# Kernel optimization log

Hardware: AMD Instinct MI355X
Metric: run time of the kernel (lower is better)

Reference implementation:

```python
import jax, jax.numpy as jnp
import numpy as np

PATCH = 16
STRIDE = 8  # patch_size - overlap

def setup_inputs() -> dict:
    key = jax.random.key(0)
    x = jax.random.normal(key, (16, 3, 512, 512), dtype=jnp.float32)
    return {"x": x, "k_neighbors": 8}

def reference(x, k_neighbors):
    B, C, H, W = x.shape
    p, s = PATCH, STRIDE
    nh = (H - p) // s + 1
    nw = (W - p) // s + 1
    N = nh * nw
    # F.unfold equivalent: feature dim ordered (C, kh, kw), then transpose(1,2)
    patches = jax.lax.conv_general_dilated_patches(
        x, filter_shape=(p, p), window_strides=(s, s), padding='VALID')  # [B, C*p*p, nh, nw]
    patches = patches.reshape(B, C * p * p, N).transpose(0, 2, 1)  # [B, N, C*p*p]
    # grid positions [(i, j)] row-major, same order as the python double loop
    ii, jj = jnp.meshgrid(jnp.arange(nh), jnp.arange(nw), indexing='ij')
    pos = jnp.stack([ii.ravel(), jj.ravel()], axis=1).astype(jnp.float32)  # [N, 2]
    positions = jnp.broadcast_to(pos[None], (B, N, 2))
    k = min(int(k_neighbors) + 1, N)
    def knn(posb):
        # squared euclidean distance preserves the ordering of cdist(p=2)
        d2 = jnp.sum((posb[:, None, :] - posb[None, :, :]) ** 2, axis=-1)  # [N, N]
        _, idx = jax.lax.top_k(-d2, k)  # k smallest distances
        tgt = idx[:, 1:]  # drop self (distance 0)
        src = jnp.broadcast_to(jnp.arange(N)[:, None], tgt.shape)
        return jnp.stack([src.ravel(), tgt.ravel()], axis=0)  # [2, N*k_neighbors]
    edge_index = jax.vmap(knn)(positions)  # [B, 2, N*k_neighbors]
    return patches, positions, edge_index
```

## Files before the change

### kernel.cpp

```cpp
#include <hip/hip_runtime.h>

#define BB      16
#define CH      3
#define HH      512
#define WW      512
#define NH      63
#define NW      63
#define NN      3969
#define FDIM    768
#define EDGES   31752

#define PATCHES_ELEMS  (BB * NN * FDIM)
#define POS_ELEMS      (BB * NN * 2)

#define PE_THREADS (BB * NN)
#define PE_BLOCKS  ((PE_THREADS + 255) / 256)
#define PATCH_BLOCKS (BB * NH)

#define PADW 516

typedef float  f4 __attribute__((ext_vector_type(4)));
typedef float  f2 __attribute__((ext_vector_type(2)));

__global__ __launch_bounds__(256) void fused_kernel(const float* __restrict__ x,
                                                    float* __restrict__ out) {
    unsigned bid = blockIdx.x;

    if (bid >= PE_BLOCKS) {
        unsigned pb = bid - PE_BLOCKS;
        unsigned b  = pb / NH;
        unsigned i  = pb % NH;
        unsigned tid = threadIdx.x;

        __shared__ float lds[16][PADW];

        unsigned lane = tid & 63u;
        unsigned wave = tid >> 6;
        unsigned dio  = lane >> 2;
        unsigned q4   = (lane & 3u) << 2;

        for (unsigned c = 0; c < CH; ++c) {
            const float* base = x + ((size_t)(b * CH + c) * HH + i * 8u) * WW;
#pragma unroll
            for (unsigned u = 0; u < 8; ++u) {
                unsigned f4id = u * 256u + tid;
                unsigned di   = f4id >> 7;
                unsigned col  = (f4id & 127u) << 2;
                *reinterpret_cast<f4*>(&lds[di][col]) =
                    *reinterpret_cast<const f4*>(base + (size_t)di * WW + col);
            }
            __syncthreads();

            for (unsigned j = wave; j < NW; j += 4) {
                const f4 v = *reinterpret_cast<const f4*>(&lds[dio][j * 8u + q4]);
                float* dst = out + ((size_t)(b * NN + i * NW + j) * FDIM
                                    + c * 256u + (lane << 2));
                __builtin_nontemporal_store(v, reinterpret_cast<f4*>(dst));
            }
            __syncthreads();
        }
    } else {
        unsigned g = bid * 256u + threadIdx.x;
        if (g >= PE_THREADS) return;
        unsigned n = g % NN;
        unsigned b = g / NN;
        int i = (int)(n / NW);
        int j = (int)(n - (unsigned)i * NW);

        *reinterpret_cast<f2*>(out + PATCHES_ELEMS + (size_t)(b * NN + n) * 2) =
            f2{(float)i, (float)j};

        unsigned best[9];
#pragma unroll
        for (int s = 0; s < 9; ++s) best[s] = 0xFFFFFFFFu;
        for (int di = -2; di <= 2; ++di) {
            int ni = i + di;
            if (ni < 0 || ni >= NH) continue;
            for (int dj = -2; dj <= 2; ++dj) {
                int nj = j + dj;
                if (nj < 0 || nj >= NW) continue;
                unsigned key = ((unsigned)(di * di + dj * dj) << 12)
                             | (unsigned)(ni * NW + nj);
#pragma unroll
                for (int s = 0; s < 9; ++s) {
                    if (key < best[s]) { unsigned tmp = best[s]; best[s] = key; key = tmp; }
                }
            }
        }

        float src_f = (float)n;
        f4 s4 = {src_f, src_f, src_f, src_f};
        f4 t0 = {(float)(best[1] & 0xFFFu), (float)(best[2] & 0xFFFu),
                 (float)(best[3] & 0xFFFu), (float)(best[4] & 0xFFFu)};
        f4 t1 = {(float)(best[5] & 0xFFFu), (float)(best[6] & 0xFFFu),
                 (float)(best[7] & 0xFFFu), (float)(best[8] & 0xFFFu)};

        float* ebase = out + PATCHES_ELEMS + POS_ELEMS + (size_t)b * 2 * EDGES;
        *reinterpret_cast<f4*>(ebase + (size_t)n * 8)             = s4;
        *reinterpret_cast<f4*>(ebase + (size_t)n * 8 + 4)         = s4;
        *reinterpret_cast<f4*>(ebase + EDGES + (size_t)n * 8)     = t0;
        *reinterpret_cast<f4*>(ebase + EDGES + (size_t)n * 8 + 4) = t1;
    }
}

extern "C" void kernel_launch(void* const* d_in, const int* in_sizes, int n_in,
                              void* d_out, int out_size, void* d_ws, size_t ws_size,
                              hipStream_t stream) {
    const float* x = (const float*)d_in[0];
    float* out     = (float*)d_out;
    fused_kernel<<<PE_BLOCKS + PATCH_BLOCKS, 256, 0, stream>>>(x, out);
}
```

Measured before the change: 238.9 us.

## Split patch blocks per channel and load rows via direct global-to-LDS

Each patch-extraction block now handles one (batch, row, channel) triple instead of looping over three channels, which triples the block count and removes the per-channel barriers. Input rows are copied straight into LDS with global_load_lds builtins, skipping the trip through registers, and the store loop is fully unrolled with a bounds check. The padded LDS row width is dropped, which may bring back bank conflicts on the strided LDS reads, and per-block setup is now repeated three times as often.

Result: faster. 232.7 us (-2.6%).

```diff
diff --git a/kernel.cpp b/kernel.cpp
--- a/kernel.cpp
+++ b/kernel.cpp
@@ -13,11 +13,9 @@
 #define PATCHES_ELEMS  (BB * NN * FDIM)
 #define POS_ELEMS      (BB * NN * 2)
 
-#define PE_THREADS (BB * NN)
-#define PE_BLOCKS  ((PE_THREADS + 255) / 256)
-#define PATCH_BLOCKS (BB * NH)
-
-#define PADW 516
+#define PE_THREADS   (BB * NN)
+#define PE_BLOCKS    ((PE_THREADS + 255) / 256)
+#define PATCH_BLOCKS (BB * NH * CH)
 
 typedef float  f4 __attribute__((ext_vector_type(4)));
 typedef float  f2 __attribute__((ext_vector_type(2)));
@@ -28,36 +26,41 @@
 
     if (bid >= PE_BLOCKS) {
         unsigned pb = bid - PE_BLOCKS;
-        unsigned b  = pb / NH;
-        unsigned i  = pb % NH;
+        unsigned c  = pb % CH;
+        unsigned bi = pb / CH;
+        unsigned i  = bi % NH;
+        unsigned b  = bi / NH;
         unsigned tid = threadIdx.x;
 
-        __shared__ float lds[16][PADW];
+        __shared__ float lds[16 * 512];
+
+        const float* base = x + ((size_t)(b * CH + c) * HH + i * 8u) * WW;
+
+        typedef const __attribute__((address_space(1))) void* gas_p;
+        typedef __attribute__((address_space(3))) void*       las_p;
+#pragma unroll
+        for (unsigned u = 0; u < 8; ++u) {
+            unsigned f4id = u * 256u + tid;
+            __builtin_amdgcn_global_load_lds((gas_p)(const void*)(base + f4id * 4u),
+                                             (las_p)(void*)(lds + f4id * 4u),
+                                             16, 0, 0);
+        }
+        __syncthreads();
 
         unsigned lane = tid & 63u;
         unsigned wave = tid >> 6;
-        unsigned dio  = lane >> 2;
-        unsigned q4   = (lane & 3u) << 2;
+        unsigned row  = (lane >> 2) << 9;
+        unsigned coff = (lane & 3u) << 2;
+        float* obase = out + ((size_t)(b * NN + i * NW) * FDIM) + c * 256u + (lane << 2);
 
-        for (unsigned c = 0; c < CH; ++c) {
-            const float* base = x + ((size_t)(b * CH + c) * HH + i * 8u) * WW;
 #pragma unroll
-            for (unsigned u = 0; u < 8; ++u) {
-                unsigned f4id = u * 256u + tid;
-                unsigned di   = f4id >> 7;
-                unsigned col  = (f4id & 127u) << 2;
-                *reinterpret_cast<f4*>(&lds[di][col]) =
-                    *reinterpret_cast<const f4*>(base + (size_t)di * WW + col);
+        for (unsigned jj = 0; jj < 16; ++jj) {
+            unsigned j = jj * 4u + wave;
+            if (j < NW) {
+                const f4 v = *reinterpret_cast<const f4*>(lds + row + j * 8u + coff);
+                __builtin_nontemporal_store(
+                    v, reinterpret_cast<f4*>(obase + (size_t)j * FDIM));
             }
-            __syncthreads();
-
-            for (unsigned j = wave; j < NW; j += 4) {
-                const f4 v = *reinterpret_cast<const f4*>(&lds[dio][j * 8u + q4]);
-                float* dst = out + ((size_t)(b * NN + i * NW + j) * FDIM
-                                    + c * 256u + (lane << 2));
-                __builtin_nontemporal_store(v, reinterpret_cast<f4*>(dst));
-            }
-            __syncthreads();
         }
     } else {
         unsigned g = bid * 256u + threadIdx.x;
```
